# Optimization experiments

Hardware: AMD Instinct MI355X
Metric: run time of the kernel (lower is better)

Reference implementation:

```python
import jax, jax.numpy as jnp
import numpy as np

B = 2048
NUM_FIELDS = 32
EMBED = 64
P = NUM_FIELDS * (NUM_FIELDS - 1) // 2  # 496 field pairs

# Pair indices (i < j), identical to the row_idx/col_idx loops in __init__
_ROW, _COL = np.triu_indices(NUM_FIELDS, k=1)
ROW_IDX = jnp.asarray(_ROW, dtype=jnp.int32)
COL_IDX = jnp.asarray(_COL, dtype=jnp.int32)


def setup_inputs() -> dict:
    key = jax.random.key(0)
    k1, k2 = jax.random.split(key)
    emb_inputs = jax.random.normal(k1, (B, NUM_FIELDS, EMBED), dtype=jnp.float32)
    # kernel_type='mat' -> kernel shape (E, P, E), xavier_normal-like init
    fan_in = P * EMBED
    fan_out = EMBED
    std = float(np.sqrt(2.0 / (fan_in + fan_out)))
    kernel = jax.random.normal(k2, (EMBED, P, EMBED), dtype=jnp.float32) * std
    return {"emb_inputs": emb_inputs, "kernel": kernel}


def reference(emb_inputs, kernel):
    # Gather field pairs: p, q shape (B, P, E)
    p = emb_inputs[:, ROW_IDX]
    q = emb_inputs[:, COL_IDX]
    # torch named-tensor chain for kernel_type='mat':
    #   kp[b, h, n] = sum_e p[b, n, e] * kernel[h, n, e]
    #   out[b, n]   = sum_h kp[b, h, n] * q[b, n, h]
    # Fused: out[b, n] = sum_{e, h} p[b, n, e] * kernel[h, n, e] * q[b, n, h]
    return jnp.einsum('bne,hne,bnh->bn', p, kernel, q)
```

## Files before the change

kernel.cpp:

```cpp
#include <hip/hip_runtime.h>


#define B_TOT 2048
#define NF    32
#define EMB   64
#define NP    496
#define BT    32
#define ESTR  72

typedef short bf16x8 __attribute__((ext_vector_type(8)));
typedef short bf16x4 __attribute__((ext_vector_type(4)));
typedef float f32x4  __attribute__((ext_vector_type(4)));

static __device__ inline unsigned f2bf(float f) {
    unsigned u = __builtin_bit_cast(unsigned, f);
    u += 0x7fffu + ((u >> 16) & 1u);
    return u >> 16;
}
static __device__ inline unsigned pack2(float lo, float hi) {
    return f2bf(lo) | (f2bf(hi) << 16);
}
static __device__ inline float bf2f(short s) {
    return __builtin_bit_cast(float, (unsigned)((unsigned short)s) << 16);
}

__global__ __launch_bounds__(256) void cvt_frag(const float* __restrict__ kern,
                                                short* __restrict__ kb) {
    const int t    = blockIdx.x * 256 + threadIdx.x;
    const int n    = t >> 9;
    const int frag = (t >> 6) & 7;
    const int l    = t & 63;
    const int h  = (frag >> 1) * 16 + (l & 15);
    const int e0 = (frag & 1) * 32 + (l >> 4) * 8;
    const float* src = kern + ((size_t)h * NP + n) * EMB + e0;
    const f32x4 a = *(const f32x4*)src;
    const f32x4 b = *(const f32x4*)(src + 4);
    uint4 w;
    w.x = pack2(a[0], a[1]); w.y = pack2(a[2], a[3]);
    w.z = pack2(b[0], b[1]); w.w = pack2(b[2], b[3]);
    *(uint4*)(kb + (size_t)t * 8) = w;
}

__global__ __launch_bounds__(512, 4) void opnl_main(
    const float* __restrict__ emb,
    const short* __restrict__ kb,
    float* __restrict__ out)
{
    __shared__ short elds[16 * BT * ESTR];

    const int g  = blockIdx.x >> 6;
    const int bt = blockIdx.x & 63;
    const int b0 = bt * BT;

    const int g2  = g - 2;
    const int oi  = (g < 2) ? 2 * g     : (g2 >> 1);
    const int oj  = (g < 2) ? 2 * g + 1 : 2 + (g2 & 1);
    const int npr = (g < 2) ? 120 : 64;

    {
        const int sb = threadIdx.x >> 4;
        const int e4 = threadIdx.x & 15;
#pragma unroll
        for (int f = 0; f < 16; ++f) {
            const int gf = (f < 8) ? oi * 8 + f : oj * 8 + (f - 8);
            const f32x4 v = *(const f32x4*)(emb + ((size_t)(b0 + sb) * NF + gf) * EMB + e4 * 4);
            uint2 w;
            w.x = pack2(v[0], v[1]);
            w.y = pack2(v[2], v[3]);
            *(uint2*)&elds[(f * BT + sb) * ESTR + e4 * 4] = w;
        }
    }
    __syncthreads();

    const int lane = threadIdx.x & 63;
    const int wid  = threadIdx.x >> 6;
    const int lo4  = lane & 15;
    const int hi4  = lane >> 4;

    for (int pi = wid; pi < npr; pi += 8) {
        int lr, lc;
        if (pi < 64) { lr = pi >> 3; lc = 8 + (pi & 7); }
        else {
            int k = pi - 64, base = 0;
            if (k >= 28) { k -= 28; base = 8; }
            int r = 0;
            while (k >= 7 - r) { k -= 7 - r; ++r; }
            lr = base + r; lc = base + r + 1 + k;
        }
        const int R = (lr < 8) ? oi * 8 + lr : oj * 8 + (lr - 8);
        const int C = (lc < 8) ? oi * 8 + lc : oj * 8 + (lc - 8);
        const int n = R * (63 - R) / 2 + (C - R - 1);

        bf16x8 wf[4][2];
        const bf16x8* wp = (const bf16x8*)(kb + (size_t)n * 4096);
#pragma unroll
        for (int mh = 0; mh < 4; ++mh)
#pragma unroll
            for (int kc = 0; kc < 2; ++kc)
                wf[mh][kc] = wp[(mh * 2 + kc) * 64 + lane];

#pragma unroll
        for (int sub = 0; sub < 2; ++sub) {
            const int bb = sub * 16 + lo4;

            bf16x8 pf[2];
#pragma unroll
            for (int kc = 0; kc < 2; ++kc)
                pf[kc] = *(const bf16x8*)&elds[(lr * BT + bb) * ESTR + kc * 32 + hi4 * 8];

            f32x4 acc[4] = {f32x4{0,0,0,0}, f32x4{0,0,0,0},
                            f32x4{0,0,0,0}, f32x4{0,0,0,0}};
#pragma unroll
            for (int mh = 0; mh < 4; ++mh)
#pragma unroll
                for (int kc = 0; kc < 2; ++kc)
                    acc[mh] = __builtin_amdgcn_mfma_f32_16x16x32_bf16(
                        wf[mh][kc], pf[kc], acc[mh], 0, 0, 0);

            float val = 0.f;
#pragma unroll
            for (int mh = 0; mh < 4; ++mh) {
                const bf16x4 q = *(const bf16x4*)&elds[(lc * BT + bb) * ESTR + mh * 16 + hi4 * 4];
                val += acc[mh][0] * bf2f(q[0]) + acc[mh][1] * bf2f(q[1])
                     + acc[mh][2] * bf2f(q[2]) + acc[mh][3] * bf2f(q[3]);
            }
            val += __shfl_xor(val, 16, 64);
            val += __shfl_xor(val, 32, 64);
            if (lane < 16) out[(size_t)(b0 + bb) * NP + n] = val;
        }
    }
}

extern "C" void kernel_launch(void* const* d_in, const int* in_sizes, int n_in,
                              void* d_out, int out_size, void* d_ws, size_t ws_size,
                              hipStream_t stream) {
    const float* emb  = (const float*)d_in[0];
    const float* kern = (const float*)d_in[1];
    float*       out  = (float*)d_out;
    short*       kb   = (short*)d_ws;

    cvt_frag<<<(NP * 512) / 256, 256, 0, stream>>>(kern, kb);

    opnl_main<<<6 * 64, 512, 0, stream>>>(emb, kb, out);
}
```

Measured before the change: 35.08 us.

## Rebalance pair work across blocks, double-buffer weights, coalesce kernel conversion

The field-pair work is repartitioned into 8 block types of 60–64 pairs each. Previously two group types carried 120 pairs against 64 for the rest, so some blocks ran nearly twice as long. Each wave now handles exactly 8 pairs in a fully unrolled loop that prefetches the next pair's bf16 weight fragments while the current pair is computed. When a type has only 60 pairs, the index wraps and a few pairs are recomputed redundantly. The weight-conversion kernel now stages each pair's slice through LDS, so global reads are contiguous rows instead of strided fragment gathers. The cost is extra register pressure from double-buffered fragments and a few duplicate stores.

```diff
diff --git a/kernel.cpp b/kernel.cpp
--- a/kernel.cpp
+++ b/kernel.cpp
@@ -24,21 +24,30 @@
     return __builtin_bit_cast(float, (unsigned)((unsigned short)s) << 16);
 }
 
-__global__ __launch_bounds__(256) void cvt_frag(const float* __restrict__ kern,
-                                                short* __restrict__ kb) {
-    const int t    = blockIdx.x * 256 + threadIdx.x;
-    const int n    = t >> 9;
-    const int frag = (t >> 6) & 7;
-    const int l    = t & 63;
-    const int h  = (frag >> 1) * 16 + (l & 15);
-    const int e0 = (frag & 1) * 32 + (l >> 4) * 8;
-    const float* src = kern + ((size_t)h * NP + n) * EMB + e0;
-    const f32x4 a = *(const f32x4*)src;
-    const f32x4 b = *(const f32x4*)(src + 4);
-    uint4 w;
-    w.x = pack2(a[0], a[1]); w.y = pack2(a[2], a[3]);
-    w.z = pack2(b[0], b[1]); w.w = pack2(b[2], b[3]);
-    *(uint4*)(kb + (size_t)t * 8) = w;
+__global__ __launch_bounds__(256) void cvt2(const float* __restrict__ kern,
+                                            short* __restrict__ kb) {
+    const int n = blockIdx.x;
+    __shared__ short w[EMB * ESTR];
+#pragma unroll
+    for (int j = 0; j < 4; ++j) {
+        const int idx = threadIdx.x + 256 * j;
+        const int h = idx >> 4, e4 = idx & 15;
+        const f32x4 v = *(const f32x4*)(kern + ((size_t)h * NP + n) * EMB + e4 * 4);
+        uint2 u;
+        u.x = pack2(v[0], v[1]);
+        u.y = pack2(v[2], v[3]);
+        *(uint2*)&w[h * ESTR + e4 * 4] = u;
+    }
+    __syncthreads();
+#pragma unroll
+    for (int j = 0; j < 2; ++j) {
+        const int u    = threadIdx.x + 256 * j;
+        const int frag = u >> 6, l = u & 63;
+        const int h  = (frag >> 1) * 16 + (l & 15);
+        const int e0 = (frag & 1) * 32 + (l >> 4) * 8;
+        const bf16x8 t = *(const bf16x8*)&w[h * ESTR + e0];
+        *(bf16x8*)(kb + (size_t)n * 4096 + u * 8) = t;
+    }
 }
 
 __global__ __launch_bounds__(512, 4) void opnl_main(
@@ -48,26 +57,31 @@
 {
     __shared__ short elds[16 * BT * ESTR];
 
-    const int g  = blockIdx.x >> 6;
-    const int bt = blockIdx.x & 63;
-    const int b0 = bt * BT;
+    const int type = blockIdx.x >> 6;
+    const int bt   = blockIdx.x & 63;
+    const int b0   = bt * BT;
 
-    const int g2  = g - 2;
-    const int oi  = (g < 2) ? 2 * g     : (g2 >> 1);
-    const int oj  = (g < 2) ? 2 * g + 1 : 2 + (g2 & 1);
-    const int npr = (g < 2) ? 120 : 64;
+    int bLo, bHi, npr;
+    switch (type) {
+        case 0: case 1: bLo = 0;  bHi = 0;  npr = 60; break;
+        case 2: case 3: bLo = 16; bHi = 16; npr = 60; break;
+        case 4:         bLo = 0;  bHi = 8;  npr = 64; break;
+        case 5:         bLo = 8;  bHi = 16; npr = 64; break;
+        case 6:         bLo = 0;  bHi = 16; npr = 64; break;
+        default:        bLo = 8;  bHi = 8;  npr = 64; break;
+    }
 
     {
         const int sb = threadIdx.x >> 4;
         const int e4 = threadIdx.x & 15;
 #pragma unroll
         for (int f = 0; f < 16; ++f) {
-            const int gf = (f < 8) ? oi * 8 + f : oj * 8 + (f - 8);
+            const int gf = f + (f < 8 ? bLo : bHi);
             const f32x4 v = *(const f32x4*)(emb + ((size_t)(b0 + sb) * NF + gf) * EMB + e4 * 4);
-            uint2 w;
-            w.x = pack2(v[0], v[1]);
-            w.y = pack2(v[2], v[3]);
-            *(uint2*)&elds[(f * BT + sb) * ESTR + e4 * 4] = w;
+            uint2 u;
+            u.x = pack2(v[0], v[1]);
+            u.y = pack2(v[2], v[3]);
+            *(uint2*)&elds[(f * BT + sb) * ESTR + e4 * 4] = u;
         }
     }
     __syncthreads();
@@ -77,28 +91,32 @@
     const int lo4  = lane & 15;
     const int hi4  = lane >> 4;
 
-    for (int pi = wid; pi < npr; pi += 8) {
-        int lr, lc;
-        if (pi < 64) { lr = pi >> 3; lc = 8 + (pi & 7); }
-        else {
-            int k = pi - 64, base = 0;
-            if (k >= 28) { k -= 28; base = 8; }
+    auto pairK = [&](int k, int& lr, int& lc, int& nn) {
+        int pr = wid + 8 * k;
+        if (pr >= npr) pr -= npr;
+        if (type < 4) {
+            int pig = (type & 1) * 60 + pr;
             int r = 0;
-            while (k >= 7 - r) { k -= 7 - r; ++r; }
-            lr = base + r; lc = base + r + 1 + k;
+            while (pig >= 15 - r) { pig -= 15 - r; ++r; }
+            lr = r; lc = r + 1 + pig;
+        } else {
+            lr = pr >> 3; lc = 8 + (pr & 7);
         }
-        const int R = (lr < 8) ? oi * 8 + lr : oj * 8 + (lr - 8);
-        const int C = (lc < 8) ? oi * 8 + lc : oj * 8 + (lc - 8);
-        const int n = R * (63 - R) / 2 + (C - R - 1);
+        const int R = lr + (lr < 8 ? bLo : bHi);
+        const int C = lc + (lc < 8 ? bLo : bHi);
+        nn = R * (63 - R) / 2 + (C - R - 1);
+    };
 
-        bf16x8 wf[4][2];
-        const bf16x8* wp = (const bf16x8*)(kb + (size_t)n * 4096);
+    auto loadW = [&](bf16x8 (&wf)[4][2], int nn) {
+        const bf16x8* wp = (const bf16x8*)(kb + (size_t)nn * 4096);
 #pragma unroll
         for (int mh = 0; mh < 4; ++mh)
 #pragma unroll
             for (int kc = 0; kc < 2; ++kc)
                 wf[mh][kc] = wp[(mh * 2 + kc) * 64 + lane];
+    };
 
+    auto compute = [&](bf16x8 (&wf)[4][2], int lr, int lc, int nn) {
 #pragma unroll
         for (int sub = 0; sub < 2; ++sub) {
             const int bb = sub * 16 + lo4;
@@ -126,7 +144,22 @@
             }
             val += __shfl_xor(val, 16, 64);
             val += __shfl_xor(val, 32, 64);
-            if (lane < 16) out[(size_t)(b0 + bb) * NP + n] = val;
+            if (lane < 16) out[(size_t)(b0 + bb) * NP + nn] = val;
+        }
+    };
+
+    bf16x8 wA[4][2], wB[4][2];
+    int lrA, lcA, nA, lrB, lcB, nB;
+    pairK(0, lrA, lcA, nA);
+    loadW(wA, nA);
+#pragma unroll
+    for (int k = 0; k < 8; ++k) {
+        if ((k & 1) == 0) {
+            if (k < 7) { pairK(k + 1, lrB, lcB, nB); loadW(wB, nB); }
+            compute(wA, lrA, lcA, nA);
+        } else {
+            if (k < 7) { pairK(k + 1, lrA, lcA, nA); loadW(wA, nA); }
+            compute(wB, lrB, lcB, nB);
         }
     }
 }
@@ -139,7 +172,6 @@
     float*       out  = (float*)d_out;
     short*       kb   = (short*)d_ws;
 
-    cvt_frag<<<(NP * 512) / 256, 256, 0, stream>>>(kern, kb);
-
-    opnl_main<<<6 * 64, 512, 0, stream>>>(emb, kb, out);
+    cvt2<<<NP, 256, 0, stream>>>(kern, kb);
+    opnl_main<<<8 * 64, 512, 0, stream>>>(emb, kb, out);
 }
```

Result: faster. 30.41 us (-13.3%).
